# Kernel tuning notes

Hardware: AMD Instinct MI355X
Metric: run time of the kernel (lower is better)

## Reference

```python
import jax, jax.numpy as jnp
import numpy as np

B, T = 256, 40
IN, E, H, V = 2048, 512, 1024, 5000


def setup_inputs() -> dict:
    key = jax.random.key(0)
    ks = jax.random.split(key, 12)
    s = 0.02
    X = jax.random.normal(ks[0], (B, IN), dtype=jnp.float32)
    labels = jax.random.randint(ks[1], (B, T), 0, V, dtype=jnp.int64)
    W_f = jax.random.normal(ks[2], (E, IN), dtype=jnp.float32) * s
    b_f = jnp.zeros((E,), dtype=jnp.float32)
    emb = jax.random.normal(ks[3], (V + 1, E), dtype=jnp.float32) * s
    emb = emb.at[V].set(0.0)  # padding_idx = vocab_size
    W_ih = jax.random.normal(ks[4], (4 * H, 2 * E), dtype=jnp.float32) * s
    W_hh = jax.random.normal(ks[5], (4 * H, H), dtype=jnp.float32) * s
    b_ih = jnp.zeros((4 * H,), dtype=jnp.float32)
    b_hh = jnp.zeros((4 * H,), dtype=jnp.float32)
    W_out = jax.random.normal(ks[6], (V, H), dtype=jnp.float32) * s
    b_out = jnp.zeros((V,), dtype=jnp.float32)
    return {"X": X, "labels": labels, "W_f": W_f, "b_f": b_f, "emb": emb,
            "W_ih": W_ih, "W_hh": W_hh, "b_ih": b_ih, "b_hh": b_hh,
            "W_out": W_out, "b_out": b_out}


def reference(X, labels, W_f, b_f, emb, W_ih, W_hh, b_ih, b_hh, W_out, b_out):
    features = X @ W_f.T + b_f                      # [B, E]
    embs = emb[labels]                              # [B, T, E]
    # step 0 uses embeddings[:, -1]; step i>0 uses embeddings[:, i-1]
    shifted = jnp.concatenate([embs[:, -1:, :], embs[:, :-1, :]], axis=1)  # [B,T,E]
    # precompute input-side gate contributions for all timesteps
    # input at step i is cat(features, shifted[:, i]) -> [B, 2E]
    gates_feat = features @ W_ih[:, :E].T           # [B, 4H], constant per step
    gates_emb = jnp.einsum('bte,ge->btg', shifted, W_ih[:, E:])  # [B, T, 4H]
    gates_x = gates_emb + (gates_feat + b_ih + b_hh)[:, None, :]  # [B, T, 4H]
    gates_x = jnp.transpose(gates_x, (1, 0, 2))     # [T, B, 4H]

    def step(carry, gx):
        h, c = carry
        g = gx + h @ W_hh.T                         # [B, 4H]
        i, f, gg, o = jnp.split(g, 4, axis=-1)      # torch LSTMCell gate order
        c = jax.nn.sigmoid(f) * c + jax.nn.sigmoid(i) * jnp.tanh(gg)
        h = jax.nn.sigmoid(o) * jnp.tanh(c)
        return (h, c), h

    h0 = jnp.zeros((X.shape[0], W_hh.shape[1]), dtype=X.dtype)
    c0 = jnp.zeros_like(h0)
    _, hs = jax.lax.scan(step, (h0, c0), gates_x)   # hs: [T, B, H]
    logits = jnp.einsum('tbh,vh->btv', hs, W_out) + b_out  # [B, T, V]
    return logits
```

## Files before the change

### kernel.cpp

```cpp
#include <hip/hip_runtime.h>
#include <hip/hip_bf16.h>
#include <math.h>

#define B_  256
#define T_  40
#define IN_ 2048
#define E_  512
#define H_  1024
#define V_  5000
#define G4_ 4096

typedef __bf16 bf16x8 __attribute__((ext_vector_type(8)));
typedef float  f32x4  __attribute__((ext_vector_type(4)));
typedef unsigned int u32x4 __attribute__((ext_vector_type(4)));

__device__ __forceinline__ float sigm_f(float x) { return 1.0f / (1.0f + __expf(-x)); }
__device__ __forceinline__ float tanh_f(float x) { return 1.0f - 2.0f / (1.0f + __expf(2.0f * x)); }

__device__ __forceinline__ unsigned short f2b(float x) {
    __hip_bfloat16 h = __float2bfloat16(x);
    return *reinterpret_cast<unsigned short*>(&h);
}
__device__ __forceinline__ float b2f(unsigned short u) {
    unsigned int v = (unsigned int)u << 16;
    return __builtin_bit_cast(float, v);
}

#define GLOAD_LDS(g, l) __builtin_amdgcn_global_load_lds(                     \
    (const __attribute__((address_space(1))) unsigned int*)(g),               \
    (__attribute__((address_space(3))) unsigned int*)(l), 16, 0, 0)

__device__ __forceinline__ void l2_load16(u32x4* dst, const unsigned short* p) {
    asm volatile("global_load_dwordx4 %0, %1, off" : "=v"(*dst) : "v"(p));
}
__device__ __forceinline__ void llc_store16(unsigned short* p, u32x4 v) {
    asm volatile("global_store_dwordx4 %0, %1, off sc0 sc1" :: "v"(p), "v"(v) : "memory");
}
__device__ __forceinline__ void llc_store4(unsigned int* p, unsigned int v) {
    asm volatile("global_store_dword %0, %1, off sc0 sc1" :: "v"(p), "v"(v) : "memory");
}
__device__ __forceinline__ unsigned int llc_load4_wait(const unsigned int* p) {
    unsigned int v;
    asm volatile("global_load_dword %0, %1, off sc0 sc1\n\ts_waitcnt vmcnt(0)"
                 : "=v"(v) : "v"(p) : "memory");
    return v;
}
#define VM_WAIT(n) do {                                                       \
    asm volatile("s_waitcnt vmcnt(" #n ")" ::: "memory");                     \
    __builtin_amdgcn_sched_barrier(0);                                        \
} while (0)

template<int OUTMODE>
__global__ __launch_bounds__(256) void gemm_mfma(
    const unsigned short* __restrict__ A, int lda, int aBlocked,
    const int* __restrict__ gidx,
    const unsigned short* __restrict__ Bm, int ldb, int bMapQ,
    const float* __restrict__ bias,
    const float* __restrict__ addMat, int rowMask, long long addStride,
    void* __restrict__ Cout, int ldc, int N, int K)
{
    __shared__ unsigned short SH[24576];

    const int tid  = threadIdx.x;
    const int wave = tid >> 6, lane = tid & 63;
    const int brow0 = blockIdx.y * 128, bcol0 = blockIdx.x * 128;
    const int wrow0 = (wave >> 1) * 64, wcol0 = (wave & 1) * 64;

    const int srow = lane >> 2;
    const int scol = (lane & 3) * 8;
    const size_t kstep = aBlocked ? 256 : 1;
    const unsigned short *pA[2], *pB[2];
    int segoff[2];
    #pragma unroll
    for (int i = 0; i < 2; ++i) {
        int seg = wave * 2 + i;
        int row = seg * 16 + srow;
        long long ar = gidx ? (long long)gidx[brow0 + row] : (long long)(brow0 + row);
        if (aBlocked)
            pA[i] = A + ((size_t)ar << 4) + ((size_t)(scol >> 4) << 12) + (scol & 8);
        else
            pA[i] = A + (size_t)ar * lda + scol;
        int bc = bcol0 + row;
        long long wrow = bMapQ ? (long long)(((bc & 3) << 10) | (bc >> 2)) : bc;
        pB[i] = Bm + wrow * ldb + scol;
        segoff[i] = seg * 512;
    }

    f32x4 acc[4][4] = {};
    const int foff = (lane & 15) * 32 + (lane >> 4) * 8;

    #define STAGE(buf, k0)                                                    \
        GLOAD_LDS(pA[0] + (size_t)(k0) * kstep, SH + (buf) * 4096 + segoff[0]); \
        GLOAD_LDS(pA[1] + (size_t)(k0) * kstep, SH + (buf) * 4096 + segoff[1]); \
        GLOAD_LDS(pB[0] + (k0), SH + 12288 + (buf) * 4096 + segoff[0]);       \
        GLOAD_LDS(pB[1] + (k0), SH + 12288 + (buf) * 4096 + segoff[1]);

    STAGE(0, 0)
    STAGE(1, 32)

    int cur = 0;
    for (int k0 = 0; k0 < K; k0 += 32) {
        if (k0 + 32 < K) { VM_WAIT(4); } else { VM_WAIT(0); }
        __builtin_amdgcn_s_barrier();

        if (k0 + 64 < K) {
            int nb = cur + 2; if (nb >= 3) nb -= 3;
            STAGE(nb, k0 + 64)
        }

        bf16x8 a[4], b[4];
        #pragma unroll
        for (int m = 0; m < 4; ++m)
            a[m] = *(const bf16x8*)&SH[cur * 4096 + (wrow0 + m * 16) * 32 + foff];
        #pragma unroll
        for (int n = 0; n < 4; ++n)
            b[n] = *(const bf16x8*)&SH[12288 + cur * 4096 + (wcol0 + n * 16) * 32 + foff];
        #pragma unroll
        for (int m = 0; m < 4; ++m)
            #pragma unroll
            for (int n = 0; n < 4; ++n)
                acc[m][n] = __builtin_amdgcn_mfma_f32_16x16x32_bf16(
                    a[m], b[n], acc[m][n], 0, 0, 0);

        ++cur; if (cur == 3) cur = 0;
    }
    #undef STAGE

    if (OUTMODE == 0) {
        #pragma unroll
        for (int m = 0; m < 4; ++m)
            #pragma unroll
            for (int j = 0; j < 4; ++j) {
                int row = brow0 + wrow0 + m * 16 + (lane >> 4) * 4 + j;
                const float* addRow = addMat
                    ? addMat + (long long)(row & rowMask) * addStride : nullptr;
                #pragma unroll
                for (int n = 0; n < 4; ++n) {
                    int col = bcol0 + wcol0 + n * 16 + (lane & 15);
                    if (col < N) {
                        float v = acc[m][n][j];
                        if (addRow) v += addRow[col];
                        if (bias)   v += bias[col];
                        ((float*)Cout)[(long long)row * ldc + col] = v;
                    }
                }
            }
    } else {
        __syncthreads();
        #pragma unroll
        for (int m = 0; m < 4; ++m)
            #pragma unroll
            for (int j = 0; j < 4; ++j) {
                int lr = wrow0 + m * 16 + (lane >> 4) * 4 + j;
                int row = brow0 + lr;
                const float* addRow = addMat + (long long)(row & rowMask) * addStride;
                #pragma unroll
                for (int n = 0; n < 4; ++n) {
                    int lc = wcol0 + n * 16 + (lane & 15);
                    SH[lr * 128 + lc] = f2b(acc[m][n][j] + addRow[bcol0 + lc]);
                }
            }
        __syncthreads();
        #pragma unroll
        for (int p = 0; p < 8; ++p) {
            int idx = p * 256 + tid;
            int lr = idx >> 4, lc8 = (idx & 15) * 8;
            *(u32x4*)((unsigned short*)Cout + (size_t)(brow0 + lr) * ldc +
                      bcol0 + lc8) = *(const u32x4*)&SH[lr * 128 + lc8];
        }
    }
}

__global__ __launch_bounds__(256) void recur_persist(
    unsigned short* __restrict__ hs,
    const unsigned short* __restrict__ Whh,
    const unsigned short* __restrict__ gates,
    unsigned int* __restrict__ flags)
{
    extern __shared__ unsigned short lds[];
    __shared__ unsigned short hstage[64][24];

    const int tid = threadIdx.x;
    const int w = tid >> 6, lane = tid & 63;
    const int mb = blockIdx.x >> 6;
    const int hb = blockIdx.x & 63;
    const int r16 = lane & 15, g4 = lane >> 4;
    const int sw7 = r16 & 7;
    const size_t SLOT = 262144;

    const int arow = mb * 64 + w * 16 + r16;
    const size_t abase = ((size_t)arow << 4) + ((g4 >> 1) << 12) + ((g4 & 1) << 3);
    const int orow0 = mb * 64 + w * 16 + g4 * 4;
    const int hc    = hb * 16 + r16;
    const int lrow0 = w * 16 + g4 * 4;
    const size_t gq_base = ((size_t)orow0 << 12) + ((size_t)hc << 2);

    ushort4 gqc[4], gqn[4];
    #pragma unroll
    for (int j = 0; j < 4; ++j)
        gqc[j] = *(const ushort4*)(gates + gq_base + ((size_t)j << 12));

    {
        const int q = w;
        for (int r = 0; r < 16; ++r) {
            const int g = q * 16 + r;
            const unsigned short* rowsrc =
                Whh + ((size_t)q * 1024 + hb * 16 + r) * H_;
            #pragma unroll
            for (int half = 0; half < 2; ++half) {
                int gran = (half * 64 + lane) ^ (g & 7);
                GLOAD_LDS(rowsrc + gran * 8, &lds[g * 1024 + half * 512]);
            }
        }
    }
    asm volatile("s_waitcnt vmcnt(0)" ::: "memory");
    __syncthreads();

    int qbase[4];
    #pragma unroll
    for (int q = 0; q < 4; ++q) qbase[q] = (q * 16 + r16) << 11;

    float cc[4];

    #define STORE_H(T1, HV)                                                   \
    {                                                                         \
        _Pragma("unroll")                                                     \
        for (int j = 0; j < 4; ++j) hstage[lrow0 + j][r16] = HV[j];           \
        __syncthreads();                                                      \
        if (w == 0) {                                                         \
            unsigned short* dst0 = hs + (size_t)(T1) * SLOT +                 \
                (((size_t)hb * 256 + mb * 64) << 4);                          \
            _Pragma("unroll")                                                 \
            for (int s = 0; s < 2; ++s) {                                     \
                int idx = s * 64 + lane;                                      \
                u32x4 v = *(const u32x4*)&hstage[idx >> 1][(idx & 1) * 8];    \
                llc_store16(dst0 + (size_t)idx * 8, v);                       \
            }                                                                 \
            asm volatile("s_waitcnt vmcnt(0)" ::: "memory");                  \
            if (lane == 0)                                                    \
                llc_store4(flags + ((T1) << 8) + (mb << 6) + hb, 1u);         \
        }                                                                     \
    }

    {
        #pragma unroll
        for (int j = 0; j < 4; ++j)
            gqn[j] = *(const ushort4*)(gates + (1ull << 20) + gq_base +
                                       ((size_t)j << 12));
        unsigned short hv[4];
        #pragma unroll
        for (int j = 0; j < 4; ++j) {
            float gi = b2f(gqc[j].x), gg = b2f(gqc[j].z), go = b2f(gqc[j].w);
            float c2 = sigm_f(gi) * tanh_f(gg);
            cc[j] = c2;
            hv[j] = f2b(sigm_f(go) * tanh_f(c2));
        }
        STORE_H(1, hv)
        #pragma unroll
        for (int j = 0; j < 4; ++j) gqc[j] = gqn[j];
    }

    for (int t = 1; t < T_; ++t) {
        {
            const unsigned int* fp = flags + ((size_t)t << 8) + (mb << 6) + lane;
            for (;;) {
                unsigned int fv = llc_load4_wait(fp);
                if (__all(fv == 1u)) break;
                __builtin_amdgcn_s_sleep(1);
            }
        }
        __builtin_amdgcn_sched_barrier(0);

        const unsigned short* hp = hs + (size_t)t * SLOT + abase;

        u32x4 a0[8], a1[8];
        #pragma unroll
        for (int u = 0; u < 8; ++u) l2_load16(&a0[u], hp + (size_t)u * 8192);
        #pragma unroll
        for (int u = 0; u < 8; ++u) l2_load16(&a1[u], hp + (size_t)(8 + u) * 8192);

        f32x4 acc[4] = {};

#define DO_CHUNK(BUF, KSB)                                                    \
        _Pragma("unroll")                                                     \
        for (int u = 0; u < 8; ++u) {                                         \
            bf16x8 a8 = __builtin_bit_cast(bf16x8, BUF[u]);                   \
            _Pragma("unroll")                                                 \
            for (int q = 0; q < 4; ++q) {                                     \
                int off = qbase[q] + (((((KSB) + u) * 4 + g4) ^ sw7) << 4);   \
                bf16x8 b8 = *(const bf16x8*)((const char*)lds + off);         \
                acc[q] = __builtin_amdgcn_mfma_f32_16x16x32_bf16(             \
                    a8, b8, acc[q], 0, 0, 0);                                 \
            }                                                                 \
        }

        VM_WAIT(8);
        DO_CHUNK(a0, 0)
        #pragma unroll
        for (int u = 0; u < 8; ++u) l2_load16(&a0[u], hp + (size_t)(16 + u) * 8192);
        VM_WAIT(8);
        DO_CHUNK(a1, 8)
        #pragma unroll
        for (int u = 0; u < 8; ++u) l2_load16(&a1[u], hp + (size_t)(24 + u) * 8192);
        VM_WAIT(8);
        DO_CHUNK(a0, 16)
        VM_WAIT(0);
        DO_CHUNK(a1, 24)
#undef DO_CHUNK

        if (t + 1 < T_) {
            #pragma unroll
            for (int j = 0; j < 4; ++j)
                gqn[j] = *(const ushort4*)(gates +
                    ((size_t)(t + 1) << 20) + gq_base + ((size_t)j << 12));
        }

        unsigned short hv[4];
        #pragma unroll
        for (int j = 0; j < 4; ++j) {
            float gi = acc[0][j] + b2f(gqc[j].x);
            float gf = acc[1][j] + b2f(gqc[j].y);
            float gg = acc[2][j] + b2f(gqc[j].z);
            float go = acc[3][j] + b2f(gqc[j].w);
            float c2 = sigm_f(gf) * cc[j] + sigm_f(gi) * tanh_f(gg);
            cc[j] = c2;
            hv[j] = f2b(sigm_f(go) * tanh_f(c2));
        }
        STORE_H(t + 1, hv)
        #pragma unroll
        for (int j = 0; j < 4; ++j) gqc[j] = gqn[j];
    }
    #undef STORE_H
}

__global__ __launch_bounds__(256) void gemm_bt(
    const float* __restrict__ A, int lda,
    const float* __restrict__ Bm, int ldb,
    const float* __restrict__ bias,
    void* __restrict__ C, int ldc, int outBF16, int N, int K)
{
    const int BK = 16;
    __shared__ float As[BK][64];
    __shared__ float Bs[BK][64];

    const int tx = threadIdx.x, ty = threadIdx.y;
    const int tid = ty * 16 + tx;
    const int brow0 = blockIdx.y * 64;
    const int bcol0 = blockIdx.x * 64;

    const int e0   = tid * 4;
    const int la_r = e0 / BK;
    const int la_k = e0 % BK;

    const long long arow_base = (long long)(brow0 + la_r) * lda;
    const int bRowG = bcol0 + la_r;
    const bool bValid = (bRowG < N);
    const long long brow_base = (long long)bRowG * ldb;

    float acc[4][4] = {};

    for (int k0 = 0; k0 < K; k0 += BK) {
        float4 av = *(const float4*)(A + arow_base + k0 + la_k);
        float4 bv = make_float4(0.f, 0.f, 0.f, 0.f);
        if (bValid) bv = *(const float4*)(Bm + brow_base + k0 + la_k);

        As[la_k + 0][la_r] = av.x; As[la_k + 1][la_r] = av.y;
        As[la_k + 2][la_r] = av.z; As[la_k + 3][la_r] = av.w;
        Bs[la_k + 0][la_r] = bv.x; Bs[la_k + 1][la_r] = bv.y;
        Bs[la_k + 2][la_r] = bv.z; Bs[la_k + 3][la_r] = bv.w;
        __syncthreads();

        #pragma unroll
        for (int kk = 0; kk < BK; ++kk) {
            float af[4], bf[4];
            #pragma unroll
            for (int i = 0; i < 4; ++i) af[i] = As[kk][ty * 4 + i];
            #pragma unroll
            for (int j = 0; j < 4; ++j) bf[j] = Bs[kk][tx * 4 + j];
            #pragma unroll
            for (int i = 0; i < 4; ++i)
                #pragma unroll
                for (int j = 0; j < 4; ++j)
                    acc[i][j] = fmaf(af[i], bf[j], acc[i][j]);
        }
        __syncthreads();
    }

    #pragma unroll
    for (int i = 0; i < 4; ++i) {
        const int row = brow0 + ty * 4 + i;
        #pragma unroll
        for (int j = 0; j < 4; ++j) {
            const int col = bcol0 + tx * 4 + j;
            if (col < N) {
                float v = acc[i][j];
                if (bias) v += bias[col];
                if (outBF16)
                    ((unsigned short*)C)[(long long)row * ldc + col] = f2b(v);
                else
                    ((float*)C)[(long long)row * ldc + col] = v;
            }
        }
    }
}

__global__ void conv2bf(const float* __restrict__ src, unsigned short* __restrict__ dst,
                        int rows, int rowsPad, int cols, int srcld, int srccol0)
{
    int i = blockIdx.x * blockDim.x + threadIdx.x;
    int c4n = cols >> 2;
    if (i >= rowsPad * c4n) return;
    int r = i / c4n, c4 = i % c4n;
    ushort4 o;
    if (r < rows) {
        float4 v = *(const float4*)(src + (long long)r * srcld + srccol0 + c4 * 4);
        o.x = f2b(v.x); o.y = f2b(v.y); o.z = f2b(v.z); o.w = f2b(v.w);
    } else {
        o = make_ushort4(0, 0, 0, 0);
    }
    *(ushort4*)(dst + (long long)r * cols + c4 * 4) = o;
}

__global__ void prep_kernel(const int* __restrict__ labels,
                            const float* __restrict__ b_ih,
                            const float* __restrict__ b_hh,
                            int* __restrict__ idxEmb,
                            int* __restrict__ idxLog,
                            float* __restrict__ bsum_perm)
{
    int r = blockIdx.x * blockDim.x + threadIdx.x;
    if (r < B_ * T_) {
        {
            int t = r >> 8, b = r & (B_ - 1);
            int tsrc = (t == 0) ? (T_ - 1) : (t - 1);
            idxEmb[r] = labels[b * T_ + tsrc];
        }
        {
            int b = r / T_, t = r % T_;
            idxLog[r] = (t + 1) * 16384 + b;
        }
    }
    if (r < G4_) {
        int w = ((r & 3) << 10) | (r >> 2);
        bsum_perm[r] = b_ih[w] + b_hh[w];
    }
}

extern "C" void kernel_launch(void* const* d_in, const int* in_sizes, int n_in,
                              void* d_out, int out_size, void* d_ws, size_t ws_size,
                              hipStream_t stream)
{
    const float* X      = (const float*)d_in[0];
    const int*   labels = (const int*)  d_in[1];
    const float* W_f    = (const float*)d_in[2];
    const float* b_f    = (const float*)d_in[3];
    const float* emb    = (const float*)d_in[4];
    const float* W_ih   = (const float*)d_in[5];
    const float* W_hh   = (const float*)d_in[6];
    const float* b_ih   = (const float*)d_in[7];
    const float* b_hh   = (const float*)d_in[8];
    const float* W_out  = (const float*)d_in[9];
    const float* b_out  = (const float*)d_in[10];
    float* out = (float*)d_out;
    (void)in_sizes; (void)n_in; (void)out_size; (void)ws_size;

    char* ws = (char*)d_ws;
    size_t off = 0;
    auto alloc = [&](size_t bytes) {
        void* p = ws + off;
        off += (bytes + 255) & ~(size_t)255;
        return p;
    };
    unsigned short* emb_bf  = (unsigned short*)alloc((size_t)(V_ + 1) * E_ * 2);
    unsigned short* WihE_bf = (unsigned short*)alloc((size_t)G4_ * E_ * 2);
    unsigned short* WihA_bf = (unsigned short*)alloc((size_t)G4_ * E_ * 2);
    unsigned short* Whh_bf  = (unsigned short*)alloc((size_t)G4_ * H_ * 2);
    unsigned short* Wout_bf = (unsigned short*)alloc((size_t)5120 * H_ * 2);
    unsigned short* hs_bf   = (unsigned short*)alloc((size_t)(T_ + 1) * 262144 * 2);
    unsigned short* feat_bf = (unsigned short*)alloc((size_t)B_ * E_ * 2);
    float* bsum_perm = (float*)alloc(G4_ * 4);
    int*   idxEmb    = (int*)  alloc(B_ * T_ * 4);
    int*   idxLog    = (int*)  alloc(B_ * T_ * 4);
    unsigned int* flags = (unsigned int*)alloc((size_t)(T_ + 1) * 256 * 4);

    unsigned short* gates_bf = (unsigned short*)out;
    float* baseMat = out + 22 * 1024 * 1024;

    hipMemsetAsync(flags, 0, (size_t)(T_ + 1) * 256 * 4, stream);

    prep_kernel<<<(B_ * T_ + 255) / 256, 256, 0, stream>>>(
        labels, b_ih, b_hh, idxEmb, idxLog, bsum_perm);

    {
        int n;
        n = (V_ + 1) * E_ / 4;
        conv2bf<<<(n + 255) / 256, 256, 0, stream>>>(emb, emb_bf, V_ + 1, V_ + 1, E_, E_, 0);
        n = G4_ * E_ / 4;
        conv2bf<<<(n + 255) / 256, 256, 0, stream>>>(W_ih, WihE_bf, G4_, G4_, E_, 2 * E_, E_);
        conv2bf<<<(n + 255) / 256, 256, 0, stream>>>(W_ih, WihA_bf, G4_, G4_, E_, 2 * E_, 0);
        n = G4_ * H_ / 4;
        conv2bf<<<(n + 255) / 256, 256, 0, stream>>>(W_hh, Whh_bf, G4_, G4_, H_, H_, 0);
        n = 5120 * H_ / 4;
        conv2bf<<<(n + 255) / 256, 256, 0, stream>>>(W_out, Wout_bf, V_, 5120, H_, H_, 0);
    }

    dim3 thr(16, 16);

    gemm_bt<<<dim3(E_ / 64, B_ / 64), thr, 0, stream>>>(
        X, IN_, W_f, IN_, b_f, feat_bf, E_, 1, E_, IN_);

    gemm_mfma<0><<<dim3(G4_ / 128, B_ / 128), 256, 0, stream>>>(
        feat_bf, E_, 0, nullptr, WihA_bf, E_, 1, nullptr,
        bsum_perm, 0, 0, baseMat, G4_, G4_, E_);

    gemm_mfma<1><<<dim3(G4_ / 128, (B_ * T_) / 128), 256, 0, stream>>>(
        emb_bf, E_, 0, idxEmb, WihE_bf, E_, 1, nullptr,
        baseMat, B_ - 1, G4_, gates_bf, G4_, G4_, E_);

    {
        hipFuncSetAttribute((const void*)recur_persist,
                            hipFuncAttributeMaxDynamicSharedMemorySize, 131072);
        recur_persist<<<256, 256, 131072, stream>>>(hs_bf, Whh_bf, gates_bf, flags);
    }

    gemm_mfma<0><<<dim3(5120 / 128, (B_ * T_) / 128), 256, 0, stream>>>(
        hs_bf, 16, 1, idxLog, Wout_bf, H_, 0, b_out,
        nullptr, 0, 0, out, V_, V_, H_);
}
```

Baseline: 718.6 us.

## Fuse prep and weight conversion kernels, re-layout gate buffer, deepen recurrent loads

Merges the index/bias prep kernel and five bf16 conversion launches into a single fused_prep kernel to cut launch overhead. The gate GEMM epilogue now writes gates in a [t][b/4][h][4 rows x 4 gates] layout so the recurrent kernel can fetch each thread's 16 gate values with two 16-byte loads instead of four 8-byte strided loads. The recurrent step issues all 32 h-vector loads up front and waits in stages, in place of reusing two 8-entry buffers. This raises register pressure in the persistent kernel and couples the GEMM output layout to the recurrent kernel's indexing.

```diff
diff --git a/kernel.cpp b/kernel.cpp
--- a/kernel.cpp
+++ b/kernel.cpp
@@ -13,6 +13,7 @@
 typedef __bf16 bf16x8 __attribute__((ext_vector_type(8)));
 typedef float  f32x4  __attribute__((ext_vector_type(4)));
 typedef unsigned int u32x4 __attribute__((ext_vector_type(4)));
+typedef unsigned short u16x8 __attribute__((ext_vector_type(8)));
 
 __device__ __forceinline__ float sigm_f(float x) { return 1.0f / (1.0f + __expf(-x)); }
 __device__ __forceinline__ float tanh_f(float x) { return 1.0f - 2.0f / (1.0f + __expf(2.0f * x)); }
@@ -161,12 +162,23 @@
                 }
             }
         __syncthreads();
-        #pragma unroll
-        for (int p = 0; p < 8; ++p) {
-            int idx = p * 256 + tid;
-            int lr = idx >> 4, lc8 = (idx & 15) * 8;
-            *(u32x4*)((unsigned short*)Cout + (size_t)(brow0 + lr) * ldc +
-                      bcol0 + lc8) = *(const u32x4*)&SH[lr * 128 + lc8];
+        const int t  = brow0 >> 8;
+        const int bq = (brow0 & 255) >> 2;
+        unsigned short* gout = (unsigned short*)Cout +
+            ((size_t)t << 20) + ((size_t)bq << 14) + ((size_t)(bcol0 >> 2) << 4);
+        #pragma unroll
+        for (int p = 0; p < 4; ++p) {
+            int cell = p * 256 + tid;
+            int rb = cell >> 5, h4 = cell & 31;
+            ushort4 r0 = *(const ushort4*)&SH[(rb * 4 + 0) * 128 + h4 * 4];
+            ushort4 r1 = *(const ushort4*)&SH[(rb * 4 + 1) * 128 + h4 * 4];
+            ushort4 r2 = *(const ushort4*)&SH[(rb * 4 + 2) * 128 + h4 * 4];
+            ushort4 r3 = *(const ushort4*)&SH[(rb * 4 + 3) * 128 + h4 * 4];
+            unsigned short* dst = gout + ((size_t)rb << 14) + ((size_t)h4 << 4);
+            u16x8 lo = {r0.x, r0.y, r0.z, r0.w, r1.x, r1.y, r1.z, r1.w};
+            u16x8 hi = {r2.x, r2.y, r2.z, r2.w, r3.x, r3.y, r3.z, r3.w};
+            *(u16x8*)(dst)     = lo;
+            *(u16x8*)(dst + 8) = hi;
         }
     }
 }
@@ -193,12 +205,11 @@
     const int orow0 = mb * 64 + w * 16 + g4 * 4;
     const int hc    = hb * 16 + r16;
     const int lrow0 = w * 16 + g4 * 4;
-    const size_t gq_base = ((size_t)orow0 << 12) + ((size_t)hc << 2);
-
-    ushort4 gqc[4], gqn[4];
-    #pragma unroll
-    for (int j = 0; j < 4; ++j)
-        gqc[j] = *(const ushort4*)(gates + gq_base + ((size_t)j << 12));
+    const size_t gq_base = ((size_t)(orow0 >> 2) << 14) + ((size_t)hc << 4);
+
+    u16x8 gA, gB, gAn, gBn;
+    gA = *(const u16x8*)(gates + gq_base);
+    gB = *(const u16x8*)(gates + gq_base + 8);
 
     {
         const int q = w;
@@ -221,6 +232,9 @@
     for (int q = 0; q < 4; ++q) qbase[q] = (q * 16 + r16) << 11;
 
     float cc[4];
+
+    #define GQV(SRC_A, SRC_B, J, Q) ((J) < 2 ? (SRC_A)[(J) * 4 + (Q)]          \
+                                             : (SRC_B)[((J) - 2) * 4 + (Q)])
 
     #define STORE_H(T1, HV)                                                   \
     {                                                                         \
@@ -243,21 +257,20 @@
     }
 
     {
-        #pragma unroll
-        for (int j = 0; j < 4; ++j)
-            gqn[j] = *(const ushort4*)(gates + (1ull << 20) + gq_base +
-                                       ((size_t)j << 12));
+        gAn = *(const u16x8*)(gates + (1ull << 20) + gq_base);
+        gBn = *(const u16x8*)(gates + (1ull << 20) + gq_base + 8);
         unsigned short hv[4];
         #pragma unroll
         for (int j = 0; j < 4; ++j) {
-            float gi = b2f(gqc[j].x), gg = b2f(gqc[j].z), go = b2f(gqc[j].w);
+            float gi = b2f(GQV(gA, gB, j, 0));
+            float gg = b2f(GQV(gA, gB, j, 2));
+            float go = b2f(GQV(gA, gB, j, 3));
             float c2 = sigm_f(gi) * tanh_f(gg);
             cc[j] = c2;
             hv[j] = f2b(sigm_f(go) * tanh_f(c2));
         }
         STORE_H(1, hv)
-        #pragma unroll
-        for (int j = 0; j < 4; ++j) gqc[j] = gqn[j];
+        gA = gAn; gB = gBn;
     }
 
     for (int t = 1; t < T_; ++t) {
@@ -273,18 +286,17 @@
 
         const unsigned short* hp = hs + (size_t)t * SLOT + abase;
 
-        u32x4 a0[8], a1[8];
-        #pragma unroll
-        for (int u = 0; u < 8; ++u) l2_load16(&a0[u], hp + (size_t)u * 8192);
-        #pragma unroll
-        for (int u = 0; u < 8; ++u) l2_load16(&a1[u], hp + (size_t)(8 + u) * 8192);
+        u32x4 av[32];
+        #pragma unroll
+        for (int u = 0; u < 32; ++u)
+            l2_load16(&av[u], hp + (size_t)u * 8192);
 
         f32x4 acc[4] = {};
 
-#define DO_CHUNK(BUF, KSB)                                                    \
+#define DO_CHUNK(KSB)                                                         \
         _Pragma("unroll")                                                     \
         for (int u = 0; u < 8; ++u) {                                         \
-            bf16x8 a8 = __builtin_bit_cast(bf16x8, BUF[u]);                   \
+            bf16x8 a8 = __builtin_bit_cast(bf16x8, av[(KSB) + u]);            \
             _Pragma("unroll")                                                 \
             for (int q = 0; q < 4; ++q) {                                     \
                 int off = qbase[q] + (((((KSB) + u) * 4 + g4) ^ sw7) << 4);   \
@@ -294,43 +306,37 @@
             }                                                                 \
         }
 
+        VM_WAIT(24);
+        DO_CHUNK(0)
+        VM_WAIT(16);
+        DO_CHUNK(8)
         VM_WAIT(8);
-        DO_CHUNK(a0, 0)
-        #pragma unroll
-        for (int u = 0; u < 8; ++u) l2_load16(&a0[u], hp + (size_t)(16 + u) * 8192);
-        VM_WAIT(8);
-        DO_CHUNK(a1, 8)
-        #pragma unroll
-        for (int u = 0; u < 8; ++u) l2_load16(&a1[u], hp + (size_t)(24 + u) * 8192);
-        VM_WAIT(8);
-        DO_CHUNK(a0, 16)
+        DO_CHUNK(16)
         VM_WAIT(0);
-        DO_CHUNK(a1, 24)
+        DO_CHUNK(24)
 #undef DO_CHUNK
 
         if (t + 1 < T_) {
-            #pragma unroll
-            for (int j = 0; j < 4; ++j)
-                gqn[j] = *(const ushort4*)(gates +
-                    ((size_t)(t + 1) << 20) + gq_base + ((size_t)j << 12));
+            gAn = *(const u16x8*)(gates + ((size_t)(t + 1) << 20) + gq_base);
+            gBn = *(const u16x8*)(gates + ((size_t)(t + 1) << 20) + gq_base + 8);
         }
 
         unsigned short hv[4];
         #pragma unroll
         for (int j = 0; j < 4; ++j) {
-            float gi = acc[0][j] + b2f(gqc[j].x);
-            float gf = acc[1][j] + b2f(gqc[j].y);
-            float gg = acc[2][j] + b2f(gqc[j].z);
-            float go = acc[3][j] + b2f(gqc[j].w);
+            float gi = acc[0][j] + b2f(GQV(gA, gB, j, 0));
+            float gf = acc[1][j] + b2f(GQV(gA, gB, j, 1));
+            float gg = acc[2][j] + b2f(GQV(gA, gB, j, 2));
+            float go = acc[3][j] + b2f(GQV(gA, gB, j, 3));
             float c2 = sigm_f(gf) * cc[j] + sigm_f(gi) * tanh_f(gg);
             cc[j] = c2;
             hv[j] = f2b(sigm_f(go) * tanh_f(c2));
         }
         STORE_H(t + 1, hv)
-        #pragma unroll
-        for (int j = 0; j < 4; ++j) gqc[j] = gqn[j];
+        gA = gAn; gB = gBn;
     }
     #undef STORE_H
+    #undef GQV
 }
 
 __global__ __launch_bounds__(256) void gemm_bt(
@@ -404,46 +410,71 @@
     }
 }
 
-__global__ void conv2bf(const float* __restrict__ src, unsigned short* __restrict__ dst,
-                        int rows, int rowsPad, int cols, int srcld, int srccol0)
+__global__ void fused_prep(
+    const float* __restrict__ emb, const float* __restrict__ W_ih,
+    const float* __restrict__ W_hh, const float* __restrict__ W_out,
+    const int* __restrict__ labels,
+    const float* __restrict__ b_ih, const float* __restrict__ b_hh,
+    unsigned short* __restrict__ emb_bf, unsigned short* __restrict__ WihE_bf,
+    unsigned short* __restrict__ WihA_bf, unsigned short* __restrict__ Whh_bf,
+    unsigned short* __restrict__ Wout_bf,
+    int* __restrict__ idxEmb, int* __restrict__ idxLog,
+    float* __restrict__ bsum_perm)
 {
-    int i = blockIdx.x * blockDim.x + threadIdx.x;
-    int c4n = cols >> 2;
-    if (i >= rowsPad * c4n) return;
-    int r = i / c4n, c4 = i % c4n;
+    const int i = blockIdx.x * 256 + threadIdx.x;
+
+    if (i < B_ * T_) {
+        {
+            int t = i >> 8, b = i & (B_ - 1);
+            int tsrc = (t == 0) ? (T_ - 1) : (t - 1);
+            idxEmb[i] = labels[b * T_ + tsrc];
+        }
+        {
+            int b = i / T_, t = i % T_;
+            idxLog[i] = (t + 1) * 16384 + b;
+        }
+    }
+    if (i < G4_) {
+        int w = ((i & 3) << 10) | (i >> 2);
+        bsum_perm[i] = b_ih[w] + b_hh[w];
+    }
+
+    const float* src = nullptr;
+    unsigned short* dst = nullptr;
+    bool zero = false;
+    if (i < 640128) {
+        int r = i >> 7, c4 = i & 127;
+        src = emb + (size_t)r * 512 + c4 * 4;
+        dst = emb_bf + (size_t)r * 512 + c4 * 4;
+    } else if (i < 1164416) {
+        int j = i - 640128, r = j >> 7, c4 = j & 127;
+        src = W_ih + (size_t)r * 1024 + 512 + c4 * 4;
+        dst = WihE_bf + (size_t)r * 512 + c4 * 4;
+    } else if (i < 1688704) {
+        int j = i - 1164416, r = j >> 7, c4 = j & 127;
+        src = W_ih + (size_t)r * 1024 + c4 * 4;
+        dst = WihA_bf + (size_t)r * 512 + c4 * 4;
+    } else if (i < 2737280) {
+        int j = i - 1688704, r = j >> 8, c4 = j & 255;
+        src = W_hh + (size_t)r * 1024 + c4 * 4;
+        dst = Whh_bf + (size_t)r * 1024 + c4 * 4;
+    } else if (i < 4048000) {
+        int j = i - 2737280, r = j >> 8, c4 = j & 255;
+        zero = (r >= V_);
+        src = W_out + (size_t)r * 1024 + c4 * 4;
+        dst = Wout_bf + (size_t)r * 1024 + c4 * 4;
+    } else {
+        return;
+    }
+
     ushort4 o;
-    if (r < rows) {
-        float4 v = *(const float4*)(src + (long long)r * srcld + srccol0 + c4 * 4);
+    if (!zero) {
+        float4 v = *(const float4*)src;
         o.x = f2b(v.x); o.y = f2b(v.y); o.z = f2b(v.z); o.w = f2b(v.w);
     } else {
         o = make_ushort4(0, 0, 0, 0);
     }
-    *(ushort4*)(dst + (long long)r * cols + c4 * 4) = o;
-}
-
-__global__ void prep_kernel(const int* __restrict__ labels,
-                            const float* __restrict__ b_ih,
-                            const float* __restrict__ b_hh,
-                            int* __restrict__ idxEmb,
-                            int* __restrict__ idxLog,
-                            float* __restrict__ bsum_perm)
-{
-    int r = blockIdx.x * blockDim.x + threadIdx.x;
-    if (r < B_ * T_) {
-        {
-            int t = r >> 8, b = r & (B_ - 1);
-            int tsrc = (t == 0) ? (T_ - 1) : (t - 1);
-            idxEmb[r] = labels[b * T_ + tsrc];
-        }
-        {
-            int b = r / T_, t = r % T_;
-            idxLog[r] = (t + 1) * 16384 + b;
-        }
-    }
-    if (r < G4_) {
-        int w = ((r & 3) << 10) | (r >> 2);
-        bsum_perm[r] = b_ih[w] + b_hh[w];
-    }
+    *(ushort4*)dst = o;
 }
 
 extern "C" void kernel_launch(void* const* d_in, const int* in_sizes, int n_in,
@@ -488,21 +519,10 @@
 
     hipMemsetAsync(flags, 0, (size_t)(T_ + 1) * 256 * 4, stream);
 
-    prep_kernel<<<(B_ * T_ + 255) / 256, 256, 0, stream>>>(
-        labels, b_ih, b_hh, idxEmb, idxLog, bsum_perm);
-
-    {
-        int n;
-        n = (V_ + 1) * E_ / 4;
-        conv2bf<<<(n + 255) / 256, 256, 0, stream>>>(emb, emb_bf, V_ + 1, V_ + 1, E_, E_, 0);
-        n = G4_ * E_ / 4;
-        conv2bf<<<(n + 255) / 256, 256, 0, stream>>>(W_ih, WihE_bf, G4_, G4_, E_, 2 * E_, E_);
-        conv2bf<<<(n + 255) / 256, 256, 0, stream>>>(W_ih, WihA_bf, G4_, G4_, E_, 2 * E_, 0);
-        n = G4_ * H_ / 4;
-        conv2bf<<<(n + 255) / 256, 256, 0, stream>>>(W_hh, Whh_bf, G4_, G4_, H_, H_, 0);
-        n = 5120 * H_ / 4;
-        conv2bf<<<(n + 255) / 256, 256, 0, stream>>>(W_out, Wout_bf, V_, 5120, H_, H_, 0);
-    }
+    fused_prep<<<(4048000 + 255) / 256, 256, 0, stream>>>(
+        emb, W_ih, W_hh, W_out, labels, b_ih, b_hh,
+        emb_bf, WihE_bf, WihA_bf, Whh_bf, Wout_bf,
+        idxEmb, idxLog, bsum_perm);
 
     dim3 thr(16, 16);
 
```

After: 720.8 us. No clear change (+0.3%).

## Fuse prep conversions, use MFMA for feature GEMM, add larger-tile output GEMM

Applied to the files above, without the earlier changes.

All fp32-to-bf16 weight and input conversions and the index/bias prep are merged into one launch, and X and W_f are now converted too. The feature projection moves from a scalar fp32 GEMM to the bf16 MFMA GEMM through a new bf16 output mode. The final vocabulary projection gets a dedicated kernel with 256x128 tiles and a three-stage global-to-LDS pipeline, meant to improve data reuse on the largest GEMM. The feature path now runs in bf16, which adds rounding error, and the new temporary buffers sit inside the output allocation.

```diff
diff --git a/kernel.cpp b/kernel.cpp
--- a/kernel.cpp
+++ b/kernel.cpp
@@ -13,6 +13,7 @@
 typedef __bf16 bf16x8 __attribute__((ext_vector_type(8)));
 typedef float  f32x4  __attribute__((ext_vector_type(4)));
 typedef unsigned int u32x4 __attribute__((ext_vector_type(4)));
+typedef unsigned short u16x8 __attribute__((ext_vector_type(8)));
 
 __device__ __forceinline__ float sigm_f(float x) { return 1.0f / (1.0f + __expf(-x)); }
 __device__ __forceinline__ float tanh_f(float x) { return 1.0f - 2.0f / (1.0f + __expf(2.0f * x)); }
@@ -145,7 +146,7 @@
                     }
                 }
             }
-    } else {
+    } else if (OUTMODE == 1) {
         __syncthreads();
         #pragma unroll
         for (int m = 0; m < 4; ++m)
@@ -168,7 +169,112 @@
             *(u32x4*)((unsigned short*)Cout + (size_t)(brow0 + lr) * ldc +
                       bcol0 + lc8) = *(const u32x4*)&SH[lr * 128 + lc8];
         }
-    }
+    } else {
+        #pragma unroll
+        for (int m = 0; m < 4; ++m)
+            #pragma unroll
+            for (int j = 0; j < 4; ++j) {
+                int row = brow0 + wrow0 + m * 16 + (lane >> 4) * 4 + j;
+                #pragma unroll
+                for (int n = 0; n < 4; ++n) {
+                    int col = bcol0 + wcol0 + n * 16 + (lane & 15);
+                    if (col < N)
+                        ((unsigned short*)Cout)[(long long)row * ldc + col] =
+                            f2b(acc[m][n][j] + (bias ? bias[col] : 0.f));
+                }
+            }
+    }
+}
+
+__global__ __launch_bounds__(256, 2) void gemm_big(
+    const unsigned short* __restrict__ A,
+    const int* __restrict__ gidx,
+    const unsigned short* __restrict__ Bm,
+    const float* __restrict__ bias,
+    float* __restrict__ C)
+{
+    __shared__ unsigned short SA[3 * 8192];
+    __shared__ unsigned short SB[3 * 4096];
+
+    const int tid = threadIdx.x;
+    const int wave = tid >> 6, lane = tid & 63;
+    const int brow0 = blockIdx.y * 256, bcol0 = blockIdx.x * 128;
+    const int wrow0 = (wave >> 1) * 128, wcol0 = (wave & 1) * 64;
+
+    const int srow = lane >> 2;
+    const int scol = (lane & 3) * 8;
+    const unsigned short* pA[4];
+    const unsigned short* pB[2];
+    int aoff[4], boff[2];
+    #pragma unroll
+    for (int i = 0; i < 4; ++i) {
+        int seg = wave * 4 + i;
+        int row = seg * 16 + srow;
+        long long ar = gidx[brow0 + row];
+        pA[i] = A + ((size_t)ar << 4) + ((size_t)(scol >> 4) << 12) + (scol & 8);
+        aoff[i] = seg * 512;
+    }
+    #pragma unroll
+    for (int i = 0; i < 2; ++i) {
+        int seg = wave * 2 + i;
+        int row = seg * 16 + srow;
+        pB[i] = Bm + (size_t)(bcol0 + row) * 1024 + scol;
+        boff[i] = seg * 512;
+    }
+
+    f32x4 acc[8][4] = {};
+    const int foff = (lane & 15) * 32 + (lane >> 4) * 8;
+
+    #define BSTAGE(buf, k0)                                                   \
+        GLOAD_LDS(pA[0] + (size_t)(k0) * 256, SA + (buf) * 8192 + aoff[0]);   \
+        GLOAD_LDS(pA[1] + (size_t)(k0) * 256, SA + (buf) * 8192 + aoff[1]);   \
+        GLOAD_LDS(pA[2] + (size_t)(k0) * 256, SA + (buf) * 8192 + aoff[2]);   \
+        GLOAD_LDS(pA[3] + (size_t)(k0) * 256, SA + (buf) * 8192 + aoff[3]);   \
+        GLOAD_LDS(pB[0] + (k0), SB + (buf) * 4096 + boff[0]);                 \
+        GLOAD_LDS(pB[1] + (k0), SB + (buf) * 4096 + boff[1]);
+
+    BSTAGE(0, 0)
+    BSTAGE(1, 32)
+
+    int cur = 0;
+    for (int k0 = 0; k0 < 1024; k0 += 32) {
+        if (k0 + 32 < 1024) { VM_WAIT(6); } else { VM_WAIT(0); }
+        __builtin_amdgcn_s_barrier();
+
+        if (k0 + 64 < 1024) {
+            int nb = cur + 2; if (nb >= 3) nb -= 3;
+            BSTAGE(nb, k0 + 64)
+        }
+
+        bf16x8 b[4];
+        #pragma unroll
+        for (int n = 0; n < 4; ++n)
+            b[n] = *(const bf16x8*)&SB[cur * 4096 + (wcol0 + n * 16) * 32 + foff];
+        #pragma unroll
+        for (int m = 0; m < 8; ++m) {
+            bf16x8 a = *(const bf16x8*)&SA[cur * 8192 + (wrow0 + m * 16) * 32 + foff];
+            #pragma unroll
+            for (int n = 0; n < 4; ++n)
+                acc[m][n] = __builtin_amdgcn_mfma_f32_16x16x32_bf16(
+                    a, b[n], acc[m][n], 0, 0, 0);
+        }
+        ++cur; if (cur == 3) cur = 0;
+    }
+    #undef BSTAGE
+
+    #pragma unroll
+    for (int m = 0; m < 8; ++m)
+        #pragma unroll
+        for (int j = 0; j < 4; ++j) {
+            int row = brow0 + wrow0 + m * 16 + (lane >> 4) * 4 + j;
+            float* orow = C + (size_t)row * 5000;
+            #pragma unroll
+            for (int n = 0; n < 4; ++n) {
+                int col = bcol0 + wcol0 + n * 16 + (lane & 15);
+                if (col < V_)
+                    orow[col] = acc[m][n][j] + bias[col];
+            }
+        }
 }
 
 __global__ __launch_bounds__(256) void recur_persist(
@@ -333,117 +439,81 @@
     #undef STORE_H
 }
 
-__global__ __launch_bounds__(256) void gemm_bt(
-    const float* __restrict__ A, int lda,
-    const float* __restrict__ Bm, int ldb,
-    const float* __restrict__ bias,
-    void* __restrict__ C, int ldc, int outBF16, int N, int K)
+__global__ void fused_prep(
+    const float* __restrict__ emb, const float* __restrict__ W_ih,
+    const float* __restrict__ W_hh, const float* __restrict__ W_out,
+    const float* __restrict__ X, const float* __restrict__ W_f,
+    const int* __restrict__ labels,
+    const float* __restrict__ b_ih, const float* __restrict__ b_hh,
+    unsigned short* __restrict__ emb_bf, unsigned short* __restrict__ WihE_bf,
+    unsigned short* __restrict__ WihA_bf, unsigned short* __restrict__ Whh_bf,
+    unsigned short* __restrict__ Wout_bf,
+    unsigned short* __restrict__ X_bf, unsigned short* __restrict__ Wf_bf,
+    int* __restrict__ idxEmb, int* __restrict__ idxLog,
+    float* __restrict__ bsum_perm)
 {
-    const int BK = 16;
-    __shared__ float As[BK][64];
-    __shared__ float Bs[BK][64];
-
-    const int tx = threadIdx.x, ty = threadIdx.y;
-    const int tid = ty * 16 + tx;
-    const int brow0 = blockIdx.y * 64;
-    const int bcol0 = blockIdx.x * 64;
-
-    const int e0   = tid * 4;
-    const int la_r = e0 / BK;
-    const int la_k = e0 % BK;
-
-    const long long arow_base = (long long)(brow0 + la_r) * lda;
-    const int bRowG = bcol0 + la_r;
-    const bool bValid = (bRowG < N);
-    const long long brow_base = (long long)bRowG * ldb;
-
-    float acc[4][4] = {};
-
-    for (int k0 = 0; k0 < K; k0 += BK) {
-        float4 av = *(const float4*)(A + arow_base + k0 + la_k);
-        float4 bv = make_float4(0.f, 0.f, 0.f, 0.f);
-        if (bValid) bv = *(const float4*)(Bm + brow_base + k0 + la_k);
-
-        As[la_k + 0][la_r] = av.x; As[la_k + 1][la_r] = av.y;
-        As[la_k + 2][la_r] = av.z; As[la_k + 3][la_r] = av.w;
-        Bs[la_k + 0][la_r] = bv.x; Bs[la_k + 1][la_r] = bv.y;
-        Bs[la_k + 2][la_r] = bv.z; Bs[la_k + 3][la_r] = bv.w;
-        __syncthreads();
-
-        #pragma unroll
-        for (int kk = 0; kk < BK; ++kk) {
-            float af[4], bf[4];
-            #pragma unroll
-            for (int i = 0; i < 4; ++i) af[i] = As[kk][ty * 4 + i];
-            #pragma unroll
-            for (int j = 0; j < 4; ++j) bf[j] = Bs[kk][tx * 4 + j];
-            #pragma unroll
-            for (int i = 0; i < 4; ++i)
-                #pragma unroll
-                for (int j = 0; j < 4; ++j)
-                    acc[i][j] = fmaf(af[i], bf[j], acc[i][j]);
-        }
-        __syncthreads();
-    }
-
-    #pragma unroll
-    for (int i = 0; i < 4; ++i) {
-        const int row = brow0 + ty * 4 + i;
-        #pragma unroll
-        for (int j = 0; j < 4; ++j) {
-            const int col = bcol0 + tx * 4 + j;
-            if (col < N) {
-                float v = acc[i][j];
-                if (bias) v += bias[col];
-                if (outBF16)
-                    ((unsigned short*)C)[(long long)row * ldc + col] = f2b(v);
-                else
-                    ((float*)C)[(long long)row * ldc + col] = v;
-            }
-        }
-    }
-}
-
-__global__ void conv2bf(const float* __restrict__ src, unsigned short* __restrict__ dst,
-                        int rows, int rowsPad, int cols, int srcld, int srccol0)
-{
-    int i = blockIdx.x * blockDim.x + threadIdx.x;
-    int c4n = cols >> 2;
-    if (i >= rowsPad * c4n) return;
-    int r = i / c4n, c4 = i % c4n;
+    const int i = blockIdx.x * 256 + threadIdx.x;
+
+    if (i < B_ * T_) {
+        {
+            int t = i >> 8, b = i & (B_ - 1);
+            int tsrc = (t == 0) ? (T_ - 1) : (t - 1);
+            idxEmb[i] = labels[b * T_ + tsrc];
+        }
+        {
+            int b = i / T_, t = i % T_;
+            idxLog[i] = (t + 1) * 16384 + b;
+        }
+    }
+    if (i < G4_) {
+        int w = ((i & 3) << 10) | (i >> 2);
+        bsum_perm[i] = b_ih[w] + b_hh[w];
+    }
+
+    const float* src = nullptr;
+    unsigned short* dst = nullptr;
+    bool zero = false;
+    if (i < 640128) {
+        int r = i >> 7, c4 = i & 127;
+        src = emb + (size_t)r * 512 + c4 * 4;
+        dst = emb_bf + (size_t)r * 512 + c4 * 4;
+    } else if (i < 1164416) {
+        int j = i - 640128, r = j >> 7, c4 = j & 127;
+        src = W_ih + (size_t)r * 1024 + 512 + c4 * 4;
+        dst = WihE_bf + (size_t)r * 512 + c4 * 4;
+    } else if (i < 1688704) {
+        int j = i - 1164416, r = j >> 7, c4 = j & 127;
+        src = W_ih + (size_t)r * 1024 + c4 * 4;
+        dst = WihA_bf + (size_t)r * 512 + c4 * 4;
+    } else if (i < 2737280) {
+        int j = i - 1688704, r = j >> 8, c4 = j & 255;
+        src = W_hh + (size_t)r * 1024 + c4 * 4;
+        dst = Whh_bf + (size_t)r * 1024 + c4 * 4;
+    } else if (i < 4048000) {
+        int j = i - 2737280, r = j >> 8, c4 = j & 255;
+        zero = (r >= V_);
+        src = W_out + (size_t)r * 1024 + c4 * 4;
+        dst = Wout_bf + (size_t)r * 1024 + c4 * 4;
+    } else if (i < 4179072) {
+        int j = i - 4048000, r = j >> 9, c4 = j & 511;
+        src = X + (size_t)r * 2048 + c4 * 4;
+        dst = X_bf + (size_t)r * 2048 + c4 * 4;
+    } else if (i < 4441216) {
+        int j = i - 4179072, r = j >> 9, c4 = j & 511;
+        src = W_f + (size_t)r * 2048 + c4 * 4;
+        dst = Wf_bf + (size_t)r * 2048 + c4 * 4;
+    } else {
+        return;
+    }
+
     ushort4 o;
-    if (r < rows) {
-        float4 v = *(const float4*)(src + (long long)r * srcld + srccol0 + c4 * 4);
+    if (!zero) {
+        float4 v = *(const float4*)src;
         o.x = f2b(v.x); o.y = f2b(v.y); o.z = f2b(v.z); o.w = f2b(v.w);
     } else {
         o = make_ushort4(0, 0, 0, 0);
     }
-    *(ushort4*)(dst + (long long)r * cols + c4 * 4) = o;
-}
-
-__global__ void prep_kernel(const int* __restrict__ labels,
-                            const float* __restrict__ b_ih,
-                            const float* __restrict__ b_hh,
-                            int* __restrict__ idxEmb,
-                            int* __restrict__ idxLog,
-                            float* __restrict__ bsum_perm)
-{
-    int r = blockIdx.x * blockDim.x + threadIdx.x;
-    if (r < B_ * T_) {
-        {
-            int t = r >> 8, b = r & (B_ - 1);
-            int tsrc = (t == 0) ? (T_ - 1) : (t - 1);
-            idxEmb[r] = labels[b * T_ + tsrc];
-        }
-        {
-            int b = r / T_, t = r % T_;
-            idxLog[r] = (t + 1) * 16384 + b;
-        }
-    }
-    if (r < G4_) {
-        int w = ((r & 3) << 10) | (r >> 2);
-        bsum_perm[r] = b_ih[w] + b_hh[w];
-    }
+    *(ushort4*)dst = o;
 }
 
 extern "C" void kernel_launch(void* const* d_in, const int* in_sizes, int n_in,
@@ -485,29 +555,19 @@
 
     unsigned short* gates_bf = (unsigned short*)out;
     float* baseMat = out + 22 * 1024 * 1024;
+    unsigned short* X_bf  = (unsigned short*)(out + 25 * 1024 * 1024);
+    unsigned short* Wf_bf = (unsigned short*)(out + 26 * 1024 * 1024);
 
     hipMemsetAsync(flags, 0, (size_t)(T_ + 1) * 256 * 4, stream);
 
-    prep_kernel<<<(B_ * T_ + 255) / 256, 256, 0, stream>>>(
-        labels, b_ih, b_hh, idxEmb, idxLog, bsum_perm);
-
-    {
-        int n;
-        n = (V_ + 1) * E_ / 4;
-        conv2bf<<<(n + 255) / 256, 256, 0, stream>>>(emb, emb_bf, V_ + 1, V_ + 1, E_, E_, 0);
-        n = G4_ * E_ / 4;
-        conv2bf<<<(n + 255) / 256, 256, 0, stream>>>(W_ih, WihE_bf, G4_, G4_, E_, 2 * E_, E_);
-        conv2bf<<<(n + 255) / 256, 256, 0, stream>>>(W_ih, WihA_bf, G4_, G4_, E_, 2 * E_, 0);
-        n = G4_ * H_ / 4;
-        conv2bf<<<(n + 255) / 256, 256, 0, stream>>>(W_hh, Whh_bf, G4_, G4_, H_, H_, 0);
-        n = 5120 * H_ / 4;
-        conv2bf<<<(n + 255) / 256, 256, 0, stream>>>(W_out, Wout_bf, V_, 5120, H_, H_, 0);
-    }
-
-    dim3 thr(16, 16);
-
-    gemm_bt<<<dim3(E_ / 64, B_ / 64), thr, 0, stream>>>(
-        X, IN_, W_f, IN_, b_f, feat_bf, E_, 1, E_, IN_);
+    fused_prep<<<(4441216 + 255) / 256, 256, 0, stream>>>(
+        emb, W_ih, W_hh, W_out, X, W_f, labels, b_ih, b_hh,
+        emb_bf, WihE_bf, WihA_bf, Whh_bf, Wout_bf, X_bf, Wf_bf,
+        idxEmb, idxLog, bsum_perm);
+
+    gemm_mfma<2><<<dim3(E_ / 128, B_ / 128), 256, 0, stream>>>(
+        X_bf, IN_, 0, nullptr, Wf_bf, IN_, 0, b_f,
+        nullptr, 0, 0, feat_bf, E_, E_, IN_);
 
     gemm_mfma<0><<<dim3(G4_ / 128, B_ / 128), 256, 0, stream>>>(
         feat_bf, E_, 0, nullptr, WihA_bf, E_, 1, nullptr,
@@ -523,7 +583,6 @@
         recur_persist<<<256, 256, 131072, stream>>>(hs_bf, Whh_bf, gates_bf, flags);
     }
 
-    gemm_mfma<0><<<dim3(5120 / 128, (B_ * T_) / 128), 256, 0, stream>>>(
-        hs_bf, 16, 1, idxLog, Wout_bf, H_, 0, b_out,
-        nullptr, 0, 0, out, V_, V_, H_);
-}
+    gemm_big<<<dim3(5120 / 128, 10240 / 256), 256, 0, stream>>>(
+        hs_bf, idxLog, Wout_bf, b_out, out);
+}
```

Result: faster. 646.6 us (median of 2 runs) (-10.0%).
